# Optimization experiments

Measured on AMD Instinct MI355X. Metric: run time of the kernel, lower is better.

Reference implementation:

```python
import jax, jax.numpy as jnp
import numpy as np

INPUT_DIM = 64
AUG_DIM = 64
STATE = INPUT_DIM + AUG_DIM  # 128
HIDDEN = 1024
T = 32
B, S = 64, 64


def setup_inputs() -> dict:
    key = jax.random.key(0)
    ks = jax.random.split(key, 12)

    def lin(kw, kb, out_d, in_d):
        scale = 1.0 / np.sqrt(in_d)
        W = jax.random.uniform(kw, (out_d, in_d), jnp.float32, -scale, scale)
        b = jax.random.uniform(kb, (out_d,), jnp.float32, -scale, scale)
        return W, b

    y0 = jax.random.normal(ks[0], (B, S, INPUT_DIM), jnp.float32)
    t = jnp.linspace(0.0, 1.0, T, dtype=jnp.float32)
    W_aug, b_aug = lin(ks[1], ks[2], AUG_DIM, INPUT_DIM)
    W0, b0 = lin(ks[3], ks[4], HIDDEN, STATE)
    W1, b1 = lin(ks[5], ks[6], HIDDEN, HIDDEN)
    W2, b2 = lin(ks[7], ks[8], HIDDEN, HIDDEN)
    W3, b3 = lin(ks[9], ks[10], STATE, HIDDEN)
    return {"y0": y0, "t": t, "W_aug": W_aug, "b_aug": b_aug,
            "W0": W0, "b0": b0, "W1": W1, "b1": b1,
            "W2": W2, "b2": b2, "W3": W3, "b3": b3}


def reference(y0, t, W_aug, b_aug, W0, b0, W1, b1, W2, b2, W3, b3):
    # augment: y0 [B,S,Din] -> [B,S,Din+Daug]
    y_aug = jnp.einsum('bsd,ad->bsa', y0, W_aug) + b_aug
    y = jnp.concatenate([y0, y_aug], axis=-1)  # [B,S,STATE]

    dt = t[1] - t[0]

    def mlp(z):
        h = jnp.tanh(jnp.einsum('bsd,hd->bsh', z, W0) + b0)
        h = jnp.tanh(jnp.einsum('bsh,gh->bsg', h, W1) + b1)
        h = jnp.tanh(jnp.einsum('bsh,gh->bsg', h, W2) + b2)
        return jnp.einsum('bsh,dh->bsd', h, W3) + b3

    def step(y_cur, _):
        y_next = y_cur + mlp(y_cur) * dt
        return y_next, None

    # forward only uses the final state: out[:, -1, :, :input_dim]
    y_final, _ = jax.lax.scan(step, y, None, length=T - 1)
    return y_final[..., :INPUT_DIM]
```

## Files before the change

### kernel.cpp

```cpp
#include <hip/hip_runtime.h>

typedef _Float16 h8 __attribute__((ext_vector_type(8)));
typedef float f32x4 __attribute__((ext_vector_type(4)));
typedef int  i4 __attribute__((ext_vector_type(4)));

#define NTHREADS 1024
#define ROWS 16
#define NBLK 256

#define SMEM_BYTES 77824

__device__ __forceinline__ float fast_tanh(float x) {
    float e = __expf(2.0f * x);
    return 1.0f - 2.0f / (e + 1.0f);
}

template<int K>
__global__ void __launch_bounds__(256) pack_kernel(const float* __restrict__ src,
                                                   _Float16* __restrict__ dst, int nfrag) {
    constexpr int NK = K / 32;
    int idx = blockIdx.x * 256 + threadIdx.x;
    if (idx >= nfrag) return;
    int lane = idx & 63;
    int ct   = (idx >> 6) & 3;
    int kk   = (idx >> 8) % NK;
    int w    = idx / (256 * NK);
    int col  = w * 64 + ct * 16 + (lane & 15);
    int kb   = kk * 32 + (lane >> 4) * 8;
    const float* s = src + (size_t)col * K + kb;
    f32x4 v0 = *(const f32x4*)s;
    f32x4 v1 = *(const f32x4*)(s + 4);
    h8 h;
    h[0]=(_Float16)v0[0]; h[1]=(_Float16)v0[1]; h[2]=(_Float16)v0[2]; h[3]=(_Float16)v0[3];
    h[4]=(_Float16)v1[0]; h[5]=(_Float16)v1[1]; h[6]=(_Float16)v1[2]; h[7]=(_Float16)v1[3];
    *(h8*)(dst + (size_t)idx * 8) = h;
}

__global__ void __launch_bounds__(256) pack8_kernel(const float* __restrict__ src,
                                                    char* __restrict__ dst, int nfrag) {
    int idx = blockIdx.x * 256 + threadIdx.x;
    if (idx >= nfrag) return;
    int lane = idx & 63;
    int ct   = (idx >> 6) & 3;
    int kk   = (idx >> 8) & 15;
    int w    = idx >> 12;
    int col  = w * 64 + ct * 16 + (lane & 15);
    int kb   = kk * 64 + (lane >> 4) * 16;
    const float* s = src + (size_t)col * 1024 + kb;
    union { char q[16]; i4 v; } u;
#pragma unroll
    for (int j = 0; j < 16; ++j)
        u.q[j] = (char)__float2int_rn(s[j] * 4064.0f);
    *(i4*)(dst + (size_t)idx * 16) = u.v;
}

__global__ void __launch_bounds__(256) pack3_kernel(const float* __restrict__ src,
                                                    _Float16* __restrict__ dst, int nfrag) {
    int idx = blockIdx.x * 256 + threadIdx.x;
    if (idx >= nfrag) return;
    int lane = idx & 63;
    int kk   = (idx >> 6) & 31;
    int w    = idx >> 11;
    int col  = w * 16 + (lane & 15);
    int kb   = kk * 32 + (lane >> 4) * 8;
    const float* s = src + (size_t)col * 1024 + kb;
    f32x4 v0 = *(const f32x4*)s;
    f32x4 v1 = *(const f32x4*)(s + 4);
    h8 h;
    h[0]=(_Float16)v0[0]; h[1]=(_Float16)v0[1]; h[2]=(_Float16)v0[2]; h[3]=(_Float16)v0[3];
    h[4]=(_Float16)v1[0]; h[5]=(_Float16)v1[1]; h[6]=(_Float16)v1[2]; h[7]=(_Float16)v1[3];
    *(h8*)(dst + (size_t)idx * 8) = h;
}

__device__ __forceinline__ void mlp0(const char* __restrict__ src, char* __restrict__ dst,
                                     const _Float16* __restrict__ Wp,
                                     const float* __restrict__ bias,
                                     int w, int l15, int lhi, int lane)
{
    constexpr int K = 128, NK = 4;
    const int colbase = w * 64;
    const _Float16* wb = Wp + (size_t)w * NK * 2048 + lane * 8;

    f32x4 acc[4];
#pragma unroll
    for (int ct = 0; ct < 4; ++ct) {
        float bv = bias[colbase + ct * 16 + l15];
        f32x4 a; a[0] = bv; a[1] = bv; a[2] = bv; a[3] = bv;
        acc[ct] = a;
    }

    h8 bE[4], bO[4], aE, aO;
    auto loadB = [&](h8* b, int kk) {
#pragma unroll
        for (int ct = 0; ct < 4; ++ct)
            b[ct] = *(const h8*)(wb + (size_t)kk * 2048 + ct * 512);
    };
    auto loadA = [&](h8& a, int kk) {
        int byte = (l15 * (2 * K) + kk * 64 + lhi * 16) ^ ((l15 & 7) << 4);
        a = *(const h8*)(src + byte);
    };
    auto mfma4 = [&](h8& a, h8* b) {
        __builtin_amdgcn_s_setprio(1);
#pragma unroll
        for (int ct = 0; ct < 4; ++ct)
            acc[ct] = __builtin_amdgcn_mfma_f32_16x16x32_f16(a, b[ct], acc[ct], 0, 0, 0);
        __builtin_amdgcn_s_setprio(0);
    };

    loadB(bE, 0); loadA(aE, 0);
    loadB(bO, 1); loadA(aO, 1);
    mfma4(aE, bE);
    loadB(bE, 2); loadA(aE, 2);
    mfma4(aO, bO);
    loadB(bO, 3); loadA(aO, 3);
    mfma4(aE, bE);
    mfma4(aO, bO);

#pragma unroll
    for (int ct = 0; ct < 4; ++ct)
#pragma unroll
        for (int j = 0; j < 4; ++j) {
            int row = lhi * 4 + j;
            int gc = colbase + ct * 16 + l15;
            int q = __float2int_rn(fast_tanh(acc[ct][j]) * 127.0f);
            int byte = (row * 1024 + gc) ^ ((row & 7) << 4);
            *(char*)(dst + byte) = (char)q;
        }
}

template<bool OUT8>
__device__ __forceinline__ void mlp8(const char* __restrict__ src, char* __restrict__ dst,
                                     const char* __restrict__ Wq,
                                     const float* __restrict__ bias,
                                     int w, int l15, int lhi, int lane)
{
    const int colbase = w * 64;
    const char* wb = Wq + (size_t)w * 65536 + lane * 16;

    i4 acc[4];
#pragma unroll
    for (int ct = 0; ct < 4; ++ct) { i4 z; z[0]=0; z[1]=0; z[2]=0; z[3]=0; acc[ct] = z; }

    i4 bE[4], bO[4], aE, aO;
    auto loadB = [&](i4* b, int kk) {
#pragma unroll
        for (int ct = 0; ct < 4; ++ct)
            b[ct] = *(const i4*)(wb + (size_t)(kk * 4 + ct) * 1024);
    };
    auto loadA = [&](i4& a, int kk) {
        int byte = (l15 * 1024 + kk * 64 + lhi * 16) ^ ((l15 & 7) << 4);
        a = *(const i4*)(src + byte);
    };
    auto mfma4 = [&](i4& a, i4* b) {
        __builtin_amdgcn_s_setprio(1);
#pragma unroll
        for (int ct = 0; ct < 4; ++ct)
            acc[ct] = __builtin_amdgcn_mfma_i32_16x16x64_i8(a, b[ct], acc[ct], 0, 0, 0);
        __builtin_amdgcn_s_setprio(0);
    };

    loadB(bE, 0); loadA(aE, 0);
#pragma unroll 1
    for (int kk2 = 0; kk2 < 7; ++kk2) {
        loadB(bO, 2 * kk2 + 1); loadA(aO, 2 * kk2 + 1);
        mfma4(aE, bE);
        loadB(bE, 2 * kk2 + 2); loadA(aE, 2 * kk2 + 2);
        mfma4(aO, bO);
    }
    loadB(bO, 15); loadA(aO, 15);
    mfma4(aE, bE);
    mfma4(aO, bO);

    const float DEQ = 1.0f / 516128.0f;
#pragma unroll
    for (int ct = 0; ct < 4; ++ct) {
        int gc = colbase + ct * 16 + l15;
        float bv = bias[gc];
#pragma unroll
        for (int j = 0; j < 4; ++j) {
            int row = lhi * 4 + j;
            float v = fast_tanh((float)acc[ct][j] * DEQ + bv);
            if constexpr (OUT8) {
                int q = __float2int_rn(v * 127.0f);
                int byte = (row * 1024 + gc) ^ ((row & 7) << 4);
                *(char*)(dst + byte) = (char)q;
            } else {
                int byte = ((row * 1024 + gc) * 2) ^ ((row & 7) << 4);
                *(_Float16*)(dst + byte) = (_Float16)v;
            }
        }
    }
}

__global__ void
__attribute__((amdgpu_flat_work_group_size(NTHREADS, NTHREADS)))
node_kernel(const float* __restrict__ y0,
            const float* __restrict__ tarr,
            const float* __restrict__ W_aug,
            const float* __restrict__ b_aug,
            const float* __restrict__ b0,
            const float* __restrict__ b1,
            const float* __restrict__ b2,
            const float* __restrict__ b3,
            const _Float16* __restrict__ W0p,
            const char* __restrict__ W1q,
            const char* __restrict__ W2q,
            const _Float16* __restrict__ W3p,
            float* __restrict__ out)
{
    __shared__ __align__(16) char smem[SMEM_BYTES];
    char* buf8A = smem;
    char* buf8B = smem + 16384;
    char* bufF  = smem + 32768;
    float* Yf   = (float*)(smem + 65536);
    char* Yh    = smem + 73728;

    const int tid  = threadIdx.x;
    const int lane = tid & 63;
    const int w    = tid >> 6;
    const int l15  = lane & 15;
    const int lhi  = lane >> 4;
    const int row0 = blockIdx.x * ROWS;

    const float dtv = tarr[1] - tarr[0];

    if (tid < 256) {
        int idx = tid * 4;
        int r = idx >> 6;
        int c = idx & 63;
        f32x4 v = *(const f32x4*)(y0 + (size_t)(row0 + r) * 64 + c);
        *(f32x4*)(Yf + r * 128 + c) = v;
    }
    __syncthreads();

    {
        int r = tid >> 6;
        int a0 = tid & 63;
        float acc = b_aug[a0];
        for (int d = 0; d < 64; ++d)
            acc += Yf[r * 128 + d] * W_aug[a0 * 64 + d];
        Yf[r * 128 + 64 + a0] = acc;
    }
    __syncthreads();

    if (tid < 256) {
        int r = tid >> 4;
        int c = (tid & 15) * 8;
        const float* p = Yf + r * 128 + c;
        h8 h;
#pragma unroll
        for (int j = 0; j < 8; ++j) h[j] = (_Float16)p[j];
        int byte = ((r * 128 + c) * 2) ^ ((r & 7) << 4);
        *(h8*)(Yh + byte) = h;
    }
    const int g = w * 16 + l15;
    f32x4 yreg;
    if (w < 8) {
#pragma unroll
        for (int j = 0; j < 4; ++j)
            yreg[j] = Yf[(lhi * 4 + j) * 128 + g];
    }
    __syncthreads();

    const _Float16* wb3 = W3p + (size_t)w * 32 * 512 + lane * 8;
    const float b3v = (w < 8) ? b3[g] : 0.0f;

    for (int s = 0; s < 31; ++s) {
        mlp0(Yh, buf8A, W0p, b0, w, l15, lhi, lane);
        __syncthreads();
        mlp8<true >(buf8A, buf8B, W1q, b1, w, l15, lhi, lane);
        __syncthreads();
        mlp8<false>(buf8B, bufF,  W2q, b2, w, l15, lhi, lane);
        __syncthreads();

        if (w < 8) {
            f32x4 acc3;
            acc3[0]=b3v; acc3[1]=b3v; acc3[2]=b3v; acc3[3]=b3v;

            h8 c3E, c3O, x3E, x3O;
            auto loadB3 = [&](h8& b, int kk) {
                b = *(const h8*)(wb3 + (size_t)kk * 512);
            };
            auto loadA3 = [&](h8& a, int kk) {
                int byte = (l15 * 2048 + kk * 64 + lhi * 16) ^ ((l15 & 7) << 4);
                a = *(const h8*)(bufF + byte);
            };

            loadB3(c3E, 0); loadA3(x3E, 0);
#pragma unroll 1
            for (int kk2 = 0; kk2 < 15; ++kk2) {
                loadB3(c3O, 2 * kk2 + 1); loadA3(x3O, 2 * kk2 + 1);
                acc3 = __builtin_amdgcn_mfma_f32_16x16x32_f16(x3E, c3E, acc3, 0, 0, 0);
                loadB3(c3E, 2 * kk2 + 2); loadA3(x3E, 2 * kk2 + 2);
                acc3 = __builtin_amdgcn_mfma_f32_16x16x32_f16(x3O, c3O, acc3, 0, 0, 0);
            }
            loadB3(c3O, 31); loadA3(x3O, 31);
            acc3 = __builtin_amdgcn_mfma_f32_16x16x32_f16(x3E, c3E, acc3, 0, 0, 0);
            acc3 = __builtin_amdgcn_mfma_f32_16x16x32_f16(x3O, c3O, acc3, 0, 0, 0);

#pragma unroll
            for (int j = 0; j < 4; ++j) {
                int row = lhi * 4 + j;
                float nv = yreg[j] + dtv * acc3[j];
                yreg[j] = nv;
                int byte = ((row * 128 + g) * 2) ^ ((row & 7) << 4);
                *(_Float16*)(Yh + byte) = (_Float16)nv;
            }
        }
        __syncthreads();
    }

    if (w < 4) {
#pragma unroll
        for (int j = 0; j < 4; ++j) {
            int row = lhi * 4 + j;
            out[(size_t)(row0 + row) * 64 + g] = yreg[j];
        }
    }
}

extern "C" void kernel_launch(void* const* d_in, const int* in_sizes, int n_in,
                              void* d_out, int out_size, void* d_ws, size_t ws_size,
                              hipStream_t stream)
{
    const float* y0    = (const float*)d_in[0];
    const float* tarr  = (const float*)d_in[1];
    const float* W_aug = (const float*)d_in[2];
    const float* b_aug = (const float*)d_in[3];
    const float* W0    = (const float*)d_in[4];
    const float* b0    = (const float*)d_in[5];
    const float* W1    = (const float*)d_in[6];
    const float* b1    = (const float*)d_in[7];
    const float* W2    = (const float*)d_in[8];
    const float* b2    = (const float*)d_in[9];
    const float* W3    = (const float*)d_in[10];
    const float* b3    = (const float*)d_in[11];

    _Float16* W0p = (_Float16*)d_ws;
    _Float16* W3p = W0p + 131072;
    char* W1q = (char*)d_ws + 524288;
    char* W2q = W1q + 1048576;

    pack_kernel<128><<<16384 / 256, 256, 0, stream>>>(W0, W0p, 16384);
    pack8_kernel<<<65536 / 256, 256, 0, stream>>>(W1, W1q, 65536);
    pack8_kernel<<<65536 / 256, 256, 0, stream>>>(W2, W2q, 65536);
    pack3_kernel<<<16384 / 256, 256, 0, stream>>>(W3, W3p, 16384);

    node_kernel<<<NBLK, NTHREADS, 0, stream>>>(y0, tarr, W_aug, b_aug,
                                               b0, b1, b2, b3,
                                               W0p, W1q, W2q, W3p,
                                               (float*)d_out);
}
```

Before: 1.452 ms.

## Quantize last layer to int8, split its K across all waves, deepen mlp8 pipeline

The final hidden-to-state layer now uses int8 weights and int8 activations with i8 MFMA instead of fp16. Its K dimension is split across two wave groups, and the partial sums are combined through an LDS reduction, so all 16 waves work on it instead of 8. The int8 hidden layers also get a deeper four-stage register prefetch with sched barriers, and the smaller activation buffer cuts LDS use. The costs are an extra barrier per step and added quantization error from int8 activations feeding the last layer.

```diff
diff --git a/kernel.cpp b/kernel.cpp
--- a/kernel.cpp
+++ b/kernel.cpp
@@ -8,7 +8,7 @@
 #define ROWS 16
 #define NBLK 256
 
-#define SMEM_BYTES 77824
+#define SMEM_BYTES 53248
 
 __device__ __forceinline__ float fast_tanh(float x) {
     float e = __expf(2.0f * x);
@@ -54,22 +54,21 @@
     *(i4*)(dst + (size_t)idx * 16) = u.v;
 }
 
-__global__ void __launch_bounds__(256) pack3_kernel(const float* __restrict__ src,
-                                                    _Float16* __restrict__ dst, int nfrag) {
+__global__ void __launch_bounds__(256) pack3q_kernel(const float* __restrict__ src,
+                                                     char* __restrict__ dst, int nfrag) {
     int idx = blockIdx.x * 256 + threadIdx.x;
     if (idx >= nfrag) return;
     int lane = idx & 63;
-    int kk   = (idx >> 6) & 31;
-    int w    = idx >> 11;
-    int col  = w * 16 + (lane & 15);
-    int kb   = kk * 32 + (lane >> 4) * 8;
+    int kk   = (idx >> 6) & 15;
+    int cg   = idx >> 10;
+    int col  = cg * 16 + (lane & 15);
+    int kb   = kk * 64 + (lane >> 4) * 16;
     const float* s = src + (size_t)col * 1024 + kb;
-    f32x4 v0 = *(const f32x4*)s;
-    f32x4 v1 = *(const f32x4*)(s + 4);
-    h8 h;
-    h[0]=(_Float16)v0[0]; h[1]=(_Float16)v0[1]; h[2]=(_Float16)v0[2]; h[3]=(_Float16)v0[3];
-    h[4]=(_Float16)v1[0]; h[5]=(_Float16)v1[1]; h[6]=(_Float16)v1[2]; h[7]=(_Float16)v1[3];
-    *(h8*)(dst + (size_t)idx * 8) = h;
+    union { char q[16]; i4 v; } u;
+#pragma unroll
+    for (int j = 0; j < 16; ++j)
+        u.q[j] = (char)__float2int_rn(s[j] * 4064.0f);
+    *(i4*)(dst + (size_t)idx * 16) = u.v;
 }
 
 __device__ __forceinline__ void mlp0(const char* __restrict__ src, char* __restrict__ dst,
@@ -77,7 +76,7 @@
                                      const float* __restrict__ bias,
                                      int w, int l15, int lhi, int lane)
 {
-    constexpr int K = 128, NK = 4;
+    constexpr int NK = 4;
     const int colbase = w * 64;
     const _Float16* wb = Wp + (size_t)w * NK * 2048 + lane * 8;
 
@@ -96,7 +95,7 @@
             b[ct] = *(const h8*)(wb + (size_t)kk * 2048 + ct * 512);
     };
     auto loadA = [&](h8& a, int kk) {
-        int byte = (l15 * (2 * K) + kk * 64 + lhi * 16) ^ ((l15 & 7) << 4);
+        int byte = (l15 * 256 + kk * 64 + lhi * 16) ^ ((l15 & 7) << 4);
         a = *(const h8*)(src + byte);
     };
     auto mfma4 = [&](h8& a, h8* b) {
@@ -128,7 +127,6 @@
         }
 }
 
-template<bool OUT8>
 __device__ __forceinline__ void mlp8(const char* __restrict__ src, char* __restrict__ dst,
                                      const char* __restrict__ Wq,
                                      const float* __restrict__ bias,
@@ -141,7 +139,9 @@
 #pragma unroll
     for (int ct = 0; ct < 4; ++ct) { i4 z; z[0]=0; z[1]=0; z[2]=0; z[3]=0; acc[ct] = z; }
 
-    i4 bE[4], bO[4], aE, aO;
+    i4 S0[4], S1[4], S2[4], S3[4];
+    i4 A0, A1, A2, A3;
+
     auto loadB = [&](i4* b, int kk) {
 #pragma unroll
         for (int ct = 0; ct < 4; ++ct)
@@ -159,17 +159,20 @@
         __builtin_amdgcn_s_setprio(0);
     };
 
-    loadB(bE, 0); loadA(aE, 0);
+    loadB(S0, 0); loadB(S1, 1); loadA(A0, 0); loadA(A1, 1);
+    __builtin_amdgcn_sched_barrier(0);
 #pragma unroll 1
-    for (int kk2 = 0; kk2 < 7; ++kk2) {
-        loadB(bO, 2 * kk2 + 1); loadA(aO, 2 * kk2 + 1);
-        mfma4(aE, bE);
-        loadB(bE, 2 * kk2 + 2); loadA(aE, 2 * kk2 + 2);
-        mfma4(aO, bO);
-    }
-    loadB(bO, 15); loadA(aO, 15);
-    mfma4(aE, bE);
-    mfma4(aO, bO);
+    for (int base = 0; base < 16; base += 4) {
+        loadB(S2, base + 2); loadB(S3, base + 3); loadA(A2, base + 2); loadA(A3, base + 3);
+        __builtin_amdgcn_sched_barrier(0);
+        mfma4(A0, S0); mfma4(A1, S1);
+        if (base + 4 < 16) {
+            loadB(S0, base + 4); loadB(S1, base + 5); loadA(A0, base + 4); loadA(A1, base + 5);
+        }
+        __builtin_amdgcn_sched_barrier(0);
+        mfma4(A2, S2); mfma4(A3, S3);
+        __builtin_amdgcn_sched_barrier(0);
+    }
 
     const float DEQ = 1.0f / 516128.0f;
 #pragma unroll
@@ -180,14 +183,9 @@
         for (int j = 0; j < 4; ++j) {
             int row = lhi * 4 + j;
             float v = fast_tanh((float)acc[ct][j] * DEQ + bv);
-            if constexpr (OUT8) {
-                int q = __float2int_rn(v * 127.0f);
-                int byte = (row * 1024 + gc) ^ ((row & 7) << 4);
-                *(char*)(dst + byte) = (char)q;
-            } else {
-                int byte = ((row * 1024 + gc) * 2) ^ ((row & 7) << 4);
-                *(_Float16*)(dst + byte) = (_Float16)v;
-            }
+            int q = __float2int_rn(v * 127.0f);
+            int byte = (row * 1024 + gc) ^ ((row & 7) << 4);
+            *(char*)(dst + byte) = (char)q;
         }
     }
 }
@@ -205,15 +203,16 @@
             const _Float16* __restrict__ W0p,
             const char* __restrict__ W1q,
             const char* __restrict__ W2q,
-            const _Float16* __restrict__ W3p,
+            const char* __restrict__ W3q,
             float* __restrict__ out)
 {
     __shared__ __align__(16) char smem[SMEM_BYTES];
     char* buf8A = smem;
     char* buf8B = smem + 16384;
-    char* bufF  = smem + 32768;
-    float* Yf   = (float*)(smem + 65536);
-    char* Yh    = smem + 73728;
+    char* buf8C = smem + 32768;
+    i4*   red   = (i4*)smem;
+    float* Yf   = (float*)(smem + 16384);
+    char* Yh    = smem + 49152;
 
     const int tid  = threadIdx.x;
     const int lane = tid & 63;
@@ -262,49 +261,58 @@
     }
     __syncthreads();
 
-    const _Float16* wb3 = W3p + (size_t)w * 32 * 512 + lane * 8;
+    const int cg  = w & 7;
+    const int kk0 = (w >> 3) * 8;
+    const char* wb3 = W3q + (size_t)cg * 16384 + lane * 16;
     const float b3v = (w < 8) ? b3[g] : 0.0f;
+    const float DEQ3 = 1.0f / 516128.0f;
 
     for (int s = 0; s < 31; ++s) {
         mlp0(Yh, buf8A, W0p, b0, w, l15, lhi, lane);
         __syncthreads();
-        mlp8<true >(buf8A, buf8B, W1q, b1, w, l15, lhi, lane);
+        mlp8(buf8A, buf8B, W1q, b1, w, l15, lhi, lane);
         __syncthreads();
-        mlp8<false>(buf8B, bufF,  W2q, b2, w, l15, lhi, lane);
+        mlp8(buf8B, buf8C, W2q, b2, w, l15, lhi, lane);
         __syncthreads();
 
-        if (w < 8) {
-            f32x4 acc3;
-            acc3[0]=b3v; acc3[1]=b3v; acc3[2]=b3v; acc3[3]=b3v;
-
-            h8 c3E, c3O, x3E, x3O;
-            auto loadB3 = [&](h8& b, int kk) {
-                b = *(const h8*)(wb3 + (size_t)kk * 512);
+        {
+            i4 acc3; acc3[0]=0; acc3[1]=0; acc3[2]=0; acc3[3]=0;
+
+            i4 c3E, c3O, x3E, x3O;
+            auto loadB3 = [&](i4& b, int kk) {
+                b = *(const i4*)(wb3 + (size_t)kk * 1024);
             };
-            auto loadA3 = [&](h8& a, int kk) {
-                int byte = (l15 * 2048 + kk * 64 + lhi * 16) ^ ((l15 & 7) << 4);
-                a = *(const h8*)(bufF + byte);
+            auto loadA3 = [&](i4& a, int kk) {
+                int byte = (l15 * 1024 + kk * 64 + lhi * 16) ^ ((l15 & 7) << 4);
+                a = *(const i4*)(buf8C + byte);
             };
 
-            loadB3(c3E, 0); loadA3(x3E, 0);
-#pragma unroll 1
-            for (int kk2 = 0; kk2 < 15; ++kk2) {
-                loadB3(c3O, 2 * kk2 + 1); loadA3(x3O, 2 * kk2 + 1);
-                acc3 = __builtin_amdgcn_mfma_f32_16x16x32_f16(x3E, c3E, acc3, 0, 0, 0);
-                loadB3(c3E, 2 * kk2 + 2); loadA3(x3E, 2 * kk2 + 2);
-                acc3 = __builtin_amdgcn_mfma_f32_16x16x32_f16(x3O, c3O, acc3, 0, 0, 0);
+            loadB3(c3E, kk0 + 0); loadA3(x3E, kk0 + 0);
+#pragma unroll
+            for (int p = 0; p < 3; ++p) {
+                loadB3(c3O, kk0 + 2 * p + 1); loadA3(x3O, kk0 + 2 * p + 1);
+                acc3 = __builtin_amdgcn_mfma_i32_16x16x64_i8(x3E, c3E, acc3, 0, 0, 0);
+                loadB3(c3E, kk0 + 2 * p + 2); loadA3(x3E, kk0 + 2 * p + 2);
+                acc3 = __builtin_amdgcn_mfma_i32_16x16x64_i8(x3O, c3O, acc3, 0, 0, 0);
             }
-            loadB3(c3O, 31); loadA3(x3O, 31);
-            acc3 = __builtin_amdgcn_mfma_f32_16x16x32_f16(x3E, c3E, acc3, 0, 0, 0);
-            acc3 = __builtin_amdgcn_mfma_f32_16x16x32_f16(x3O, c3O, acc3, 0, 0, 0);
-
-#pragma unroll
-            for (int j = 0; j < 4; ++j) {
-                int row = lhi * 4 + j;
-                float nv = yreg[j] + dtv * acc3[j];
-                yreg[j] = nv;
-                int byte = ((row * 128 + g) * 2) ^ ((row & 7) << 4);
-                *(_Float16*)(Yh + byte) = (_Float16)nv;
+            loadB3(c3O, kk0 + 7); loadA3(x3O, kk0 + 7);
+            acc3 = __builtin_amdgcn_mfma_i32_16x16x64_i8(x3E, c3E, acc3, 0, 0, 0);
+            acc3 = __builtin_amdgcn_mfma_i32_16x16x64_i8(x3O, c3O, acc3, 0, 0, 0);
+
+            if (w >= 8)
+                red[cg * 64 + lane] = acc3;
+            __syncthreads();
+            if (w < 8) {
+                i4 part = red[w * 64 + lane];
+#pragma unroll
+                for (int j = 0; j < 4; ++j) {
+                    int row = lhi * 4 + j;
+                    float dy = (float)(acc3[j] + part[j]) * DEQ3 + b3v;
+                    float nv = yreg[j] + dtv * dy;
+                    yreg[j] = nv;
+                    int byte = ((row * 128 + g) * 2) ^ ((row & 7) << 4);
+                    *(_Float16*)(Yh + byte) = (_Float16)nv;
+                }
             }
         }
         __syncthreads();
@@ -337,17 +345,17 @@
     const float* b3    = (const float*)d_in[11];
 
     _Float16* W0p = (_Float16*)d_ws;
-    _Float16* W3p = W0p + 131072;
-    char* W1q = (char*)d_ws + 524288;
-    char* W2q = W1q + 1048576;
+    char* W1q = (char*)d_ws + 262144;
+    char* W2q = (char*)d_ws + 1310720;
+    char* W3q = (char*)d_ws + 2359296;
 
     pack_kernel<128><<<16384 / 256, 256, 0, stream>>>(W0, W0p, 16384);
     pack8_kernel<<<65536 / 256, 256, 0, stream>>>(W1, W1q, 65536);
     pack8_kernel<<<65536 / 256, 256, 0, stream>>>(W2, W2q, 65536);
-    pack3_kernel<<<16384 / 256, 256, 0, stream>>>(W3, W3p, 16384);
+    pack3q_kernel<<<8192 / 256, 256, 0, stream>>>(W3, W3q, 8192);
 
     node_kernel<<<NBLK, NTHREADS, 0, stream>>>(y0, tarr, W_aug, b_aug,
                                                b0, b1, b2, b3,
-                                               W0p, W1q, W2q, W3p,
+                                               W0p, W1q, W2q, W3q,
                                                (float*)d_out);
 }
```

After: 2.329 ms. +60.4%, slower.
